# Optimization experiments

Hardware: AMD Instinct MI355X
Metric: run time of the kernel (lower is better)

Reference implementation:

```python
import jax, jax.numpy as jnp
import numpy as np

B = 64            # graphs
N0 = 1024         # nodes per graph at level 0
DEG = 16          # avg degree
D = 128
NS = [1024, 820, 656, 525, 420, 336]  # ceil(0.8*n) cascade


def gcn(x, src, dst, valid, W, b, num_nodes):
    # x: [N,D]; src/dst: [E] int; valid: [E] float mask; W: [D,D]; b: [D]
    x = x @ W.T + b
    deg = jax.ops.segment_sum(valid, src, num_segments=num_nodes) + 1.0  # +1 self loop
    dis = jax.lax.rsqrt(deg)
    norm = dis[src] * dis[dst] * valid
    agg = jax.ops.segment_sum(norm[:, None] * x[src], dst, num_segments=num_nodes)
    return agg + (dis * dis)[:, None] * x  # self-loop term


def topk_pool(x, src, dst, valid, w, n, k):
    # PyG TopKPooling: score = tanh((x.w)/||w||); keep top ceil(ratio*n) per graph
    s = jnp.tanh((x @ w) / jnp.linalg.norm(w))
    _, idx = jax.lax.top_k(s.reshape(B, n), k)                    # [B,k] local ids
    perm = (idx + (jnp.arange(B) * n)[:, None]).reshape(-1)       # global ids
    xn = x[perm] * s[perm][:, None]
    new_id = jnp.full((B * n,), -1, jnp.int32).at[perm].set(jnp.arange(B * k, dtype=jnp.int32))
    ns_, nd_ = new_id[src], new_id[dst]
    v = valid * ((ns_ >= 0) & (nd_ >= 0)).astype(jnp.float32)
    return xn, jnp.maximum(ns_, 0), jnp.maximum(nd_, 0), v


def setup_inputs() -> dict:
    key = jax.random.key(0)
    ks = jax.random.split(key, 32)
    x = jax.random.normal(ks[0], (B * N0, D), jnp.float32)
    eg = N0 * DEG  # edges per graph
    local = jax.random.randint(ks[1], (2, B, eg), 0, N0, jnp.int32)
    edge_index = (local + (jnp.arange(B, dtype=jnp.int32) * N0)[None, :, None]).reshape(2, -1)
    batch = jnp.repeat(jnp.arange(B, dtype=jnp.int32), N0)
    sc = 1.0 / np.sqrt(D)
    inp = {"x": x, "edge_index": edge_index, "batch": batch}
    for i in range(1, 6):
        inp[f"c{i}w"] = jax.random.normal(ks[2 * i], (D, D), jnp.float32) * sc
        inp[f"c{i}b"] = jnp.zeros((D,), jnp.float32)
        inp[f"p{i}w"] = jax.random.normal(ks[2 * i + 1], (D,), jnp.float32) * sc
    inp["l1w"] = jax.random.normal(ks[20], (128, 256), jnp.float32) / np.sqrt(256)
    inp["l1b"] = jnp.zeros((128,), jnp.float32)
    inp["l2w"] = jax.random.normal(ks[21], (64, 128), jnp.float32) * sc
    inp["l2b"] = jnp.zeros((64,), jnp.float32)
    inp["l3w"] = jax.random.normal(ks[22], (2, 64), jnp.float32) / np.sqrt(64)
    inp["l3b"] = jnp.zeros((2,), jnp.float32)
    return inp


def reference(x, edge_index, batch,
              c1w, c1b, p1w, c2w, c2b, p2w, c3w, c3b, p3w,
              c4w, c4b, p4w, c5w, c5b, p5w,
              l1w, l1b, l2w, l2b, l3w, l3b):
    src, dst = edge_index[0], edge_index[1]
    valid = jnp.ones(src.shape, jnp.float32)
    layers = [(c1w, c1b, p1w), (c2w, c2b, p2w), (c3w, c3b, p3w),
              (c4w, c4b, p4w), (c5w, c5b, p5w)]
    reads = []
    for i, (cw, cb, pw) in enumerate(layers):
        n, k = NS[i], NS[i + 1]
        x = jax.nn.relu(gcn(x, src, dst, valid, cw, cb, B * n))
        x, src, dst, valid = topk_pool(x, src, dst, valid, pw, n, k)
        xk = x.reshape(B, k, D)
        reads.append(jnp.concatenate([xk.max(axis=1), xk.mean(axis=1)], axis=1))
    h = reads[0] + reads[1] + reads[2] + reads[3] + reads[4]   # [B,256]
    h = jax.nn.relu(h @ l1w.T + l1b)
    # dropout is identity in eval mode
    h = jax.nn.relu(h @ l2w.T + l2b)
    return jax.nn.log_softmax(h @ l3w.T + l3b, axis=-1)       # [B,2]
```

## Files before the change

kernel.cpp:

```cpp
#include <hip/hip_runtime.h>
#include <hip/hip_fp16.h>
#include <math.h>

#define NB 64
#define DIM 128
#define ETOT 1048576
#define EPG 16384
#define EPT 16

static const int NS_H[6] = {1024, 820, 656, 525, 420, 336};

typedef _Float16 f16x8 __attribute__((ext_vector_type(8)));
typedef float f32x4 __attribute__((ext_vector_type(4)));
typedef float f32x2 __attribute__((ext_vector_type(2)));
typedef unsigned short ushortT;

__device__ __forceinline__ unsigned fxform(float f) {
    int b = __float_as_int(f);
    return (b >= 0) ? ((unsigned)b | 0x80000000u) : ~(unsigned)b;
}
__device__ __forceinline__ float fxinv(unsigned u) {
    int b = (u & 0x80000000u) ? (int)(u ^ 0x80000000u) : (int)~u;
    return __int_as_float(b);
}
__device__ __forceinline__ unsigned hmax2u(unsigned a, unsigned b) {
    float2 fa = __half22float2(*(__half2*)&a);
    float2 fb = __half22float2(*(__half2*)&b);
    __half2 r = __floats2half2_rn(fmaxf(fa.x, fb.x), fmaxf(fa.y, fb.y));
    return *(unsigned*)&r;
}
__device__ __forceinline__ unsigned hadd2u(unsigned a, unsigned b) {
    float2 fa = __half22float2(*(__half2*)&a);
    float2 fb = __half22float2(*(__half2*)&b);
    __half2 r = __floats2half2_rn(fa.x + fb.x, fa.y + fb.y);
    return *(unsigned*)&r;
}

__global__ __launch_bounds__(1024) void init_kernel(const int* __restrict__ ei,
                                  unsigned* __restrict__ sd,
                                  ushortT* __restrict__ eidx, int* __restrict__ eoff,
                                  int* __restrict__ cnt, float* __restrict__ dinv,
                                  float* __restrict__ invn, const float* __restrict__ pw0,
                                  unsigned* __restrict__ maxb, float* __restrict__ sumb,
                                  const float* __restrict__ cw0, const float* __restrict__ cw1,
                                  const float* __restrict__ cw2, const float* __restrict__ cw3,
                                  const float* __restrict__ cw4, __half* __restrict__ W16) {
    __shared__ int hs[1024], hc[1024], cur[1024];
    __shared__ float dv[1024];
    __shared__ float shf[128];
    __shared__ int wsum[16];
    int g = blockIdx.x, t = threadIdx.x;
    int lane = t & 63, wv = t >> 6;
    hs[t] = 0; hc[t] = 0;
    int idx = g * 1024 + t;
    if (idx < 5 * NB * 128) { maxb[idx] = 0x007FFFFFu; sumb[idx] = 0.f; }
    if (g < 5) {
        const float* wsrc = (g == 0) ? cw0 : (g == 1) ? cw1 : (g == 2) ? cw2
                           : (g == 3) ? cw3 : cw4;
        for (int i = t; i < 16384; i += 1024)
            W16[g * 16384 + i] = __float2half(wsrc[i]);
    }
    __syncthreads();
    int b0 = g * EPG;
    int sr[EPT], dr[EPT];
#pragma unroll
    for (int q = 0; q < EPT; q++) {
        int e = b0 + q * 1024 + t;
        int s = ei[e] & 1023, d = ei[ETOT + e] & 1023;
        sr[q] = s; dr[q] = d;
        sd[e] = ((unsigned)d << 16) | (unsigned)s;
        atomicAdd(&hs[s], 1);
        atomicAdd(&hc[d], 1);
    }
    __syncthreads();
    int v = hc[t];
    dv[t] = rsqrtf((float)hs[t] + 1.0f);
    int s = v;
#pragma unroll
    for (int off = 1; off < 64; off <<= 1) {
        int u = __shfl_up(s, off, 64);
        if (lane >= off) s += u;
    }
    if (lane == 63) wsum[wv] = s;
    __syncthreads();
    if (wv == 0) {
        int ws = (lane < 16) ? wsum[lane] : 0;
#pragma unroll
        for (int off = 1; off < 16; off <<= 1) {
            int u = __shfl_up(ws, off, 64);
            if (lane >= off) ws += u;
        }
        if (lane < 16) wsum[lane] = ws;
    }
    __syncthreads();
    int excl = b0 + s + ((wv > 0) ? wsum[wv - 1] : 0) - v;
    eoff[g * 1024 + t] = excl;
    cnt[g * 1024 + t] = v;
    dinv[g * 1024 + t] = dv[t];
    cur[t] = excl;
    __syncthreads();
#pragma unroll
    for (int q = 0; q < EPT; q++) {
        int pos = atomicAdd(&cur[dr[q]], 1);
        eidx[pos] = (ushortT)(g * 1024 + sr[q]);
    }
    if (g == 0) {
        if (t < 128) shf[t] = pw0[t] * pw0[t];
        __syncthreads();
        for (int q = 64; q > 0; q >>= 1) {
            if (t < q) shf[t] += shf[t + q];
            __syncthreads();
        }
        if (t == 0) invn[0] = rsqrtf(shf[0]);
    }
}

__global__ __launch_bounds__(256) void linear_kernel(const float* __restrict__ x,
                              const __half* __restrict__ xA,
                              const int* __restrict__ perm, const float* __restrict__ sval,
                              const __half* __restrict__ W16, const float* __restrict__ b,
                              const float* __restrict__ dinvL,
                              __half* __restrict__ xH,
                              unsigned* __restrict__ maxbL, float* __restrict__ sumbL,
                              int n_prev, int kk, int cpg, int mode) {
    __shared__ float rmaxW[512], rsumW[512];
    int tid = threadIdx.x;
    int g   = blockIdx.x / cpg;
    int j0  = (blockIdx.x % cpg) * 64;
    int wv  = tid >> 6;
    int l   = tid & 63;
    int l16 = l & 15;
    int kgrp = l >> 4;
    int jrow = j0 + wv * 16 + l16;
    bool valid = jrow < kk;
    f16x8 bf[4];
    if (mode) {
        int idx = g * kk + (valid ? jrow : 0);
        int rowg = perm[idx];
        float sc = valid ? sval[idx] : 0.f;
        const uint4* xrow = (const uint4*)(xA + (size_t)(g * n_prev + rowg) * DIM);
#pragma unroll
        for (int kb = 0; kb < 4; kb++) {
            uint4 hv = xrow[kb * 4 + kgrp];
            __half2* hp = (__half2*)&hv;
#pragma unroll
            for (int q = 0; q < 4; q++) {
                float2 f = __half22float2(hp[q]);
                hp[q] = __floats2half2_rn(f.x * sc, f.y * sc);
            }
            bf[kb] = *(f16x8*)&hv;
        }
    } else {
        const float* xrow = x + (size_t)(g * kk + jrow) * DIM;
#pragma unroll
        for (int kb = 0; kb < 4; kb++) {
            float4 a = *(const float4*)(xrow + kb * 32 + kgrp * 8);
            float4 c = *(const float4*)(xrow + kb * 32 + kgrp * 8 + 4);
            __half2 h0 = __floats2half2_rn(a.x, a.y), h1 = __floats2half2_rn(a.z, a.w);
            __half2 h2 = __floats2half2_rn(c.x, c.y), h3 = __floats2half2_rn(c.z, c.w);
            uint4 hv;
            hv.x = *(unsigned*)&h0; hv.y = *(unsigned*)&h1;
            hv.z = *(unsigned*)&h2; hv.w = *(unsigned*)&h3;
            bf[kb] = *(f16x8*)&hv;
        }
    }
    if (mode) {
#pragma unroll
        for (int kb = 0; kb < 4; kb++) {
            uint4 fv = *(uint4*)&bf[kb];
            uint4 mxv, smv;
            if (valid) { mxv = fv; smv = fv; }
            else {
                mxv = make_uint4(0xFC00FC00u, 0xFC00FC00u, 0xFC00FC00u, 0xFC00FC00u);
                smv = make_uint4(0u, 0u, 0u, 0u);
            }
#pragma unroll
            for (int st = 1; st < 16; st <<= 1) {
                uint4 om, os;
                om.x = __shfl_xor(mxv.x, st, 16); om.y = __shfl_xor(mxv.y, st, 16);
                om.z = __shfl_xor(mxv.z, st, 16); om.w = __shfl_xor(mxv.w, st, 16);
                os.x = __shfl_xor(smv.x, st, 16); os.y = __shfl_xor(smv.y, st, 16);
                os.z = __shfl_xor(smv.z, st, 16); os.w = __shfl_xor(smv.w, st, 16);
                mxv.x = hmax2u(mxv.x, om.x); mxv.y = hmax2u(mxv.y, om.y);
                mxv.z = hmax2u(mxv.z, om.z); mxv.w = hmax2u(mxv.w, om.w);
                smv.x = hadd2u(smv.x, os.x); smv.y = hadd2u(smv.y, os.y);
                smv.z = hadd2u(smv.z, os.z); smv.w = hadd2u(smv.w, os.w);
            }
            if (l16 == 0) {
                int cb = wv * 128 + kb * 32 + kgrp * 8;
                __half2* mh = (__half2*)&mxv;
                __half2* sh = (__half2*)&smv;
#pragma unroll
                for (int q = 0; q < 4; q++) {
                    float2 fm = __half22float2(mh[q]);
                    float2 fs = __half22float2(sh[q]);
                    rmaxW[cb + q * 2 + 0] = fm.x; rmaxW[cb + q * 2 + 1] = fm.y;
                    rsumW[cb + q * 2 + 0] = fs.x; rsumW[cb + q * 2 + 1] = fs.y;
                }
            }
        }
    }
    f32x4 acc[8];
#pragma unroll
    for (int ft = 0; ft < 8; ft++) {
        float4 bv = *(const float4*)(b + ft * 16 + kgrp * 4);
        f32x4 a; a[0] = bv.x; a[1] = bv.y; a[2] = bv.z; a[3] = bv.w;
        acc[ft] = a;
    }
    const uint4* wp = (const uint4*)W16;
#pragma unroll
    for (int kb = 0; kb < 4; kb++) {
#pragma unroll
        for (int ft = 0; ft < 8; ft++) {
            uint4 wfrag = wp[(ft * 16 + l16) * 16 + kb * 4 + kgrp];
            acc[ft] = __builtin_amdgcn_mfma_f32_16x16x32_f16(*(f16x8*)&wfrag, bf[kb],
                                                             acc[ft], 0, 0, 0);
        }
    }
    if (valid) {
        float dsn = dinvL[g * kk + jrow];
        __half* yrow = xH + (size_t)(g * kk + jrow) * DIM;
#pragma unroll
        for (int ft = 0; ft < 8; ft++) {
            __half2 h0 = __floats2half2_rn(acc[ft][0] * dsn, acc[ft][1] * dsn);
            __half2 h1 = __floats2half2_rn(acc[ft][2] * dsn, acc[ft][3] * dsn);
            uint2 pk;
            pk.x = *(unsigned*)&h0; pk.y = *(unsigned*)&h1;
            *(uint2*)(yrow + ft * 16 + kgrp * 4) = pk;
        }
    }
    if (mode) {
        __syncthreads();
        if (tid < 128) {
            float m = rmaxW[tid], s = rsumW[tid];
#pragma unroll
            for (int w = 1; w < 4; w++) {
                m = fmaxf(m, rmaxW[w * 128 + tid]);
                s += rsumW[w * 128 + tid];
            }
            atomicMax(&maxbL[g * 128 + tid], fxform(m));
            atomicAdd(&sumbL[g * 128 + tid], s);
        }
    }
}

#define ACC8(xv) { \
    float2 c0_ = __half22float2(*(const __half2*)&(xv).x); \
    float2 c1_ = __half22float2(*(const __half2*)&(xv).y); \
    float2 c2_ = __half22float2(*(const __half2*)&(xv).z); \
    float2 c3_ = __half22float2(*(const __half2*)&(xv).w); \
    a0[0] += c0_.x; a0[1] += c0_.y; a1[0] += c1_.x; a1[1] += c1_.y; \
    a2[0] += c2_.x; a2[1] += c2_.y; a3[0] += c3_.x; a3[1] += c3_.y; }

__global__ __launch_bounds__(256, 4) void fused_agg_kernel(
                                 const __half* __restrict__ xH, const ushortT* __restrict__ eidx,
                                 const int* __restrict__ eoff, const int* __restrict__ cnt,
                                 const float* __restrict__ dinv,
                                 const float* __restrict__ pw, const float* __restrict__ invn,
                                 __half* __restrict__ xA, float* __restrict__ score, int n) {
    int t = threadIdx.x;
    int g = blockIdx.x % NB;
    int chunk = blockIdx.x / NB;
    int ln = chunk * 8 + (t >> 5);
    if (ln >= n) return;
    int node = g * n + ln;
    int lane = t & 31;
    int sub = lane & 15;
    int hi  = lane >> 4;
    const uint4* __restrict__ xr = (const uint4*)xH;
    float dsn = dinv[node];
    f32x2 a0 = {0.f, 0.f}, a1 = {0.f, 0.f}, a2 = {0.f, 0.f}, a3 = {0.f, 0.f};
    if (!hi) {
        uint4 qs = xr[(unsigned)node * 16u + sub];
        ACC8(qs);
    }
    int s0 = eoff[node], s1 = s0 + cnt[node];
    int j = s0;
    while ((j & 3) && j < s1) {
        if (!hi) {
            uint4 xv = xr[(unsigned)eidx[j] * 16u + sub];
            ACC8(xv);
        }
        j++;
    }
    int nq = (s1 - j) >> 2;
    int rem = (s1 - j) & 3;
    const uint2* __restrict__ e4 = (const uint2*)(eidx + j);
    int q = 0;
    while (nq >= 2) {
        uint2 D0 = e4[q], D1 = e4[q + 1];
        unsigned r0 = hi ? (D0.x >> 16) : (D0.x & 0xFFFFu);
        unsigned r1 = hi ? (D0.y >> 16) : (D0.y & 0xFFFFu);
        unsigned r2 = hi ? (D1.x >> 16) : (D1.x & 0xFFFFu);
        unsigned r3 = hi ? (D1.y >> 16) : (D1.y & 0xFFFFu);
        uint4 x0 = xr[r0 * 16u + sub];
        uint4 x1 = xr[r1 * 16u + sub];
        uint4 x2 = xr[r2 * 16u + sub];
        uint4 x3 = xr[r3 * 16u + sub];
        ACC8(x0); ACC8(x1); ACC8(x2); ACC8(x3);
        q += 2; nq -= 2;
    }
    if (nq == 1) {
        uint2 D0 = e4[q];
        unsigned r0 = hi ? (D0.x >> 16) : (D0.x & 0xFFFFu);
        unsigned r1 = hi ? (D0.y >> 16) : (D0.y & 0xFFFFu);
        uint4 x0 = xr[r0 * 16u + sub];
        uint4 x1 = xr[r1 * 16u + sub];
        ACC8(x0); ACC8(x1);
    }
    for (int e = s1 - rem; e < s1; e++) {
        if (!hi) {
            uint4 xv = xr[(unsigned)eidx[e] * 16u + sub];
            ACC8(xv);
        }
    }
    float acc0 = a0[0], acc1 = a0[1], acc2 = a1[0], acc3 = a1[1];
    float acc4 = a2[0], acc5 = a2[1], acc6 = a3[0], acc7 = a3[1];
    acc0 += __shfl_xor(acc0, 16, 32); acc1 += __shfl_xor(acc1, 16, 32);
    acc2 += __shfl_xor(acc2, 16, 32); acc3 += __shfl_xor(acc3, 16, 32);
    acc4 += __shfl_xor(acc4, 16, 32); acc5 += __shfl_xor(acc5, 16, 32);
    acc6 += __shfl_xor(acc6, 16, 32); acc7 += __shfl_xor(acc7, 16, 32);
    acc0 = fmaxf(acc0 * dsn, 0.f); acc1 = fmaxf(acc1 * dsn, 0.f);
    acc2 = fmaxf(acc2 * dsn, 0.f); acc3 = fmaxf(acc3 * dsn, 0.f);
    acc4 = fmaxf(acc4 * dsn, 0.f); acc5 = fmaxf(acc5 * dsn, 0.f);
    acc6 = fmaxf(acc6 * dsn, 0.f); acc7 = fmaxf(acc7 * dsn, 0.f);
    if (!hi) {
        __half2 h0 = __floats2half2_rn(acc0, acc1);
        __half2 h1 = __floats2half2_rn(acc2, acc3);
        __half2 h2 = __floats2half2_rn(acc4, acc5);
        __half2 h3 = __floats2half2_rn(acc6, acc7);
        uint4 pk;
        pk.x = *(unsigned int*)&h0; pk.y = *(unsigned int*)&h1;
        pk.z = *(unsigned int*)&h2; pk.w = *(unsigned int*)&h3;
        ((uint4*)xA)[(unsigned)node * 16u + sub] = pk;
    }
    float4 pa = ((const float4*)pw)[sub * 2];
    float4 pb = ((const float4*)pw)[sub * 2 + 1];
    float dot = acc0 * pa.x + acc1 * pa.y + acc2 * pa.z + acc3 * pa.w
              + acc4 * pb.x + acc5 * pb.y + acc6 * pb.z + acc7 * pb.w;
#pragma unroll
    for (int off = 8; off >= 1; off >>= 1) dot += __shfl_xor(dot, off, 16);
    if (lane == 0) score[node] = tanhf(dot * invn[0]);
}

__global__ __launch_bounds__(1024) void pool_kernel(const float* __restrict__ score,
                              int* __restrict__ permG, float* __restrict__ svalG,
                              unsigned* __restrict__ sd,
                              ushortT* __restrict__ eidx, int* __restrict__ eoff,
                              int* __restrict__ cnt, float* __restrict__ dinv,
                              const float* __restrict__ pwN, float* __restrict__ invn,
                              const __half* __restrict__ xA,
                              const unsigned* __restrict__ maxb, const float* __restrict__ sumb,
                              const float* __restrict__ l1w, const float* __restrict__ l1b,
                              const float* __restrict__ l2w, const float* __restrict__ l2b,
                              const float* __restrict__ l3w, const float* __restrict__ l3b,
                              float* __restrict__ out,
                              int n, int k, int last) {
    __shared__ float keyS[2][1024];
    __shared__ int idxS[2][1024];
    __shared__ int nid[1024];
    __shared__ int hs[1024], hc[1024], cur[1024];
    __shared__ float dv[1024];
    __shared__ float shf[128];
    __shared__ int wsum[16];
    __shared__ float4 smax[32][33], ssm[32][33];
    __shared__ float hr[256], h1[128], h2[64], lz[2];
    int g = blockIdx.x, t = threadIdx.x;
    int lane = t & 63, wv = t >> 6;
    int b0 = g * EPG, gk = g * k;
    float k_r = (t < n) ? score[g * n + t] : -2.0f;
    int i_r = t;
    hs[t] = 0; hc[t] = 0;
    unsigned sde[EPT];
    if (!last) {
#pragma unroll
        for (int q = 0; q < EPT; q++) {
            int e = b0 + q * 1024 + t;
            sde[q] = sd[e];
        }
    }
    int par = 0;
    for (unsigned ksz = 2; ksz <= 1024; ksz <<= 1) {
        for (unsigned jj = ksz >> 1; jj > 0; jj >>= 1) {
            float kq; int iq;
            if (jj >= 64) {
                keyS[par][t] = k_r; idxS[par][t] = i_r;
                __syncthreads();
                kq = keyS[par][t ^ jj]; iq = idxS[par][t ^ jj];
                par ^= 1;
            } else {
                kq = __shfl_xor(k_r, (int)jj, 64);
                iq = __shfl_xor(i_r, (int)jj, 64);
            }
            bool mineFirst = (k_r > kq) || (k_r == kq && i_r < iq);
            bool up = ((t & ksz) == 0);
            bool iAmLower = ((t & jj) == 0);
            bool keepMine = (iAmLower == up) ? mineFirst : !mineFirst;
            if (!keepMine) { k_r = kq; i_r = iq; }
        }
    }
    nid[i_r] = (t < (unsigned)k) ? t : -1;
    keyS[0][t] = k_r; idxS[0][t] = i_r;
    if (!last && t < k) { permG[gk + t] = i_r; svalG[gk + t] = k_r; }
    __syncthreads();
    if (last) {
        int lane4 = t & 31, ch = t >> 5;
        float4 mx = make_float4(-INFINITY, -INFINITY, -INFINITY, -INFINITY);
        float4 sm = make_float4(0.f, 0.f, 0.f, 0.f);
        for (int j = ch; j < k; j += 32) {
            int row = idxS[0][j];
            float sv = keyS[0][j];
            uint2 hv = ((const uint2*)(xA + ((size_t)(g * n + row)) * DIM))[lane4];
            float2 lo = __half22float2(*(const __half2*)&hv.x);
            float2 hi2 = __half22float2(*(const __half2*)&hv.y);
            float4 vv = make_float4(lo.x * sv, lo.y * sv, hi2.x * sv, hi2.y * sv);
            mx.x = fmaxf(mx.x, vv.x); mx.y = fmaxf(mx.y, vv.y);
            mx.z = fmaxf(mx.z, vv.z); mx.w = fmaxf(mx.w, vv.w);
            sm.x += vv.x; sm.y += vv.y; sm.z += vv.z; sm.w += vv.w;
        }
        smax[ch][lane4] = mx;
        ssm[ch][lane4] = sm;
        __syncthreads();
        for (int s2 = 16; s2 >= 1; s2 >>= 1) {
            if (ch < s2) {
                float4 a = smax[ch][lane4], bb = smax[ch + s2][lane4];
                a.x = fmaxf(a.x, bb.x); a.y = fmaxf(a.y, bb.y);
                a.z = fmaxf(a.z, bb.z); a.w = fmaxf(a.w, bb.w);
                smax[ch][lane4] = a;
                float4 c = ssm[ch][lane4], d = ssm[ch + s2][lane4];
                c.x += d.x; c.y += d.y; c.z += d.z; c.w += d.w;
                ssm[ch][lane4] = c;
            }
            __syncthreads();
        }
        if (t < 128) {
            const float invk[4] = {1.f / 820.f, 1.f / 656.f, 1.f / 525.f, 1.f / 420.f};
            float mxs = ((const float*)&smax[0][t >> 2])[t & 3];
            float sms = ((const float*)&ssm[0][t >> 2])[t & 3] * (1.f / 336.f);
#pragma unroll
            for (int L = 0; L < 4; L++) {
                mxs += fxinv(maxb[(L * NB + g) * 128 + t]);
                sms += sumb[(L * NB + g) * 128 + t] * invk[L];
            }
            hr[t] = mxs;
            hr[128 + t] = sms;
        }
        __syncthreads();
        if (t < 128) {
            float a1 = l1b[t];
            for (int d = 0; d < 256; d++) a1 += hr[d] * l1w[t * 256 + d];
            h1[t] = fmaxf(a1, 0.f);
        }
        __syncthreads();
        if (t < 64) {
            float a2 = l2b[t];
            for (int d = 0; d < 128; d++) a2 += h1[d] * l2w[t * 128 + d];
            h2[t] = fmaxf(a2, 0.f);
        }
        __syncthreads();
        if (t < 2) {
            float a3 = l3b[t];
            for (int d = 0; d < 64; d++) a3 += h2[d] * l3w[t * 64 + d];
            lz[t] = a3;
        }
        __syncthreads();
        if (t < 2) {
            float z0 = lz[0], z1 = lz[1];
            float m = fmaxf(z0, z1);
            float lse = m + logf(expf(z0 - m) + expf(z1 - m));
            out[g * 2 + t] = lz[t] - lse;
        }
        return;
    }
    int sr[EPT], dr[EPT];
#pragma unroll
    for (int q = 0; q < EPT; q++) {
        int e = b0 + q * 1024 + t;
        unsigned v = sde[q];
        int s2 = -1, d2 = -1;
        if (v != 0xFFFFFFFFu) {
            int sl = (int)(v & 0xFFFFu), dl = (int)(v >> 16);
            s2 = nid[sl];
            d2 = nid[dl];
            if (s2 >= 0 && d2 >= 0) {
                sd[e] = ((unsigned)d2 << 16) | (unsigned)s2;
                atomicAdd(&hs[s2], 1);
                atomicAdd(&hc[d2], 1);
            } else {
                sd[e] = 0xFFFFFFFFu;
                s2 = -1;
            }
        }
        sr[q] = s2; dr[q] = d2;
    }
    __syncthreads();
    int v = (t < k) ? hc[t] : 0;
    if (t < k) dv[t] = rsqrtf((float)hs[t] + 1.0f);
    int s = v;
#pragma unroll
    for (int off = 1; off < 64; off <<= 1) {
        int u = __shfl_up(s, off, 64);
        if (lane >= off) s += u;
    }
    if (lane == 63) wsum[wv] = s;
    __syncthreads();
    if (wv == 0) {
        int ws = (lane < 16) ? wsum[lane] : 0;
#pragma unroll
        for (int off = 1; off < 16; off <<= 1) {
            int u = __shfl_up(ws, off, 64);
            if (lane >= off) ws += u;
        }
        if (lane < 16) wsum[lane] = ws;
    }
    __syncthreads();
    if (t < k) {
        int excl = b0 + s + ((wv > 0) ? wsum[wv - 1] : 0) - v;
        eoff[gk + t] = excl;
        cnt[gk + t] = v;
        dinv[gk + t] = dv[t];
        cur[t] = excl;
    }
    __syncthreads();
#pragma unroll
    for (int q = 0; q < EPT; q++) {
        if (sr[q] >= 0) {
            int pos = atomicAdd(&cur[dr[q]], 1);
            eidx[pos] = (ushortT)(gk + sr[q]);
        }
    }
    if (g == 0) {
        if (t < 128) shf[t] = pwN[t] * pwN[t];
        __syncthreads();
        for (int q = 64; q > 0; q >>= 1) {
            if (t < q) shf[t] += shf[t + q];
            __syncthreads();
        }
        if (t == 0) invn[0] = rsqrtf(shf[0]);
    }
}

extern "C" void kernel_launch(void* const* d_in, const int* in_sizes, int n_in,
                              void* d_out, int out_size, void* d_ws, size_t ws_size,
                              hipStream_t stream) {
    const float* x_in = (const float*)d_in[0];
    const int* edge_index = (const int*)d_in[1];
    const float *cw[5], *cb[5], *pw[5];
    for (int i = 0; i < 5; i++) {
        cw[i] = (const float*)d_in[3 + 3 * i];
        cb[i] = (const float*)d_in[4 + 3 * i];
        pw[i] = (const float*)d_in[5 + 3 * i];
    }
    const float* l1w = (const float*)d_in[18];
    const float* l1b = (const float*)d_in[19];
    const float* l2w = (const float*)d_in[20];
    const float* l2b = (const float*)d_in[21];
    const float* l3w = (const float*)d_in[22];
    const float* l3b = (const float*)d_in[23];
    float* out = (float*)d_out;

    char* w = (char*)d_ws;
    __half* xA    = (__half*)w; w += (size_t)65536 * DIM * 2;
    __half* xH    = (__half*)w; w += (size_t)65536 * DIM * 2;
    unsigned* sd  = (unsigned*)w; w += (size_t)ETOT * 4;
    ushortT* eidx = (ushortT*)w; w += (size_t)ETOT * 2;
    int*   cnt   = (int*)w;   w += (size_t)65536 * 4;
    int*   eoff  = (int*)w;   w += (size_t)65536 * 4;
    float* dinv  = (float*)w; w += (size_t)65536 * 4;
    float* score = (float*)w; w += (size_t)65536 * 4;
    int*   perm  = (int*)w;   w += (size_t)65536 * 4;
    float* sval  = (float*)w; w += (size_t)65536 * 4;
    unsigned* maxb = (unsigned*)w; w += (size_t)5 * NB * 128 * 4;
    float* sumb  = (float*)w; w += (size_t)5 * NB * 128 * 4;
    __half* W16  = (__half*)w; w += (size_t)5 * 16384 * 2;
    float* invn  = (float*)w; w += 4;

    init_kernel<<<NB, 1024, 0, stream>>>(edge_index, sd, eidx, eoff, cnt, dinv,
                                         invn, pw[0], maxb, sumb,
                                         cw[0], cw[1], cw[2], cw[3], cw[4], W16);

    for (int i = 0; i < 5; i++) {
        int n = NS_H[i], k = NS_H[i + 1];
        int cpg = (n + 63) / 64;
        int last = (i == 4) ? 1 : 0;

        linear_kernel<<<NB * cpg, 256, 0, stream>>>(
            x_in, xA, perm, sval, W16 + (size_t)i * 16384, cb[i], dinv, xH,
            (i > 0) ? maxb + (size_t)(i - 1) * NB * 128 : (unsigned*)maxb,
            (i > 0) ? sumb + (size_t)(i - 1) * NB * 128 : (float*)sumb,
            (i > 0) ? NS_H[i - 1] : 0, n, cpg, (i > 0) ? 1 : 0);

        int gpb = (n + 7) / 8;
        fused_agg_kernel<<<NB * gpb, 256, 0, stream>>>(xH, eidx, eoff, cnt, dinv, pw[i],
                                                       invn, xA, score, n);
        pool_kernel<<<NB, 1024, 0, stream>>>(score, perm, sval, sd, eidx, eoff,
                                             cnt, dinv, (i < 4) ? pw[i + 1] : pw[i], invn,
                                             xA, maxb, sumb,
                                             l1w, l1b, l2w, l2b, l3w, l3b, out,
                                             n, k, last);
    }
}
```

Baseline: 442.5 us.

## Merge linear and aggregation kernels into one cooperative kernel with grid sync

Combines the per-layer linear (MFMA) kernel and the neighbour aggregation kernel into a single cooperative launch with grid-stride loops, separated by a grid-wide barrier. This removes one kernel launch and its launch gap per layer. In exchange the grid is capped at occupancy-limited size (up to 2048 blocks), so work runs in persistent loops. There is also a hazard: the aggregation phase writes xA while the linear phase of the same launch reads it, but the grid sync orders the two phases.

Result: slower. 1.278 ms (+188.8%).

```diff
diff --git a/kernel.cpp b/kernel.cpp
--- a/kernel.cpp
+++ b/kernel.cpp
@@ -1,6 +1,9 @@
 #include <hip/hip_runtime.h>
+#include <hip/hip_cooperative_groups.h>
 #include <hip/hip_fp16.h>
 #include <math.h>
+
+namespace cg = cooperative_groups;
 
 #define NB 64
 #define DIM 128
@@ -115,134 +118,26 @@
     }
 }
 
-__global__ __launch_bounds__(256) void linear_kernel(const float* __restrict__ x,
-                              const __half* __restrict__ xA,
-                              const int* __restrict__ perm, const float* __restrict__ sval,
-                              const __half* __restrict__ W16, const float* __restrict__ b,
-                              const float* __restrict__ dinvL,
-                              __half* __restrict__ xH,
-                              unsigned* __restrict__ maxbL, float* __restrict__ sumbL,
-                              int n_prev, int kk, int cpg, int mode) {
-    __shared__ float rmaxW[512], rsumW[512];
-    int tid = threadIdx.x;
-    int g   = blockIdx.x / cpg;
-    int j0  = (blockIdx.x % cpg) * 64;
-    int wv  = tid >> 6;
-    int l   = tid & 63;
-    int l16 = l & 15;
-    int kgrp = l >> 4;
-    int jrow = j0 + wv * 16 + l16;
-    bool valid = jrow < kk;
-    f16x8 bf[4];
-    if (mode) {
-        int idx = g * kk + (valid ? jrow : 0);
-        int rowg = perm[idx];
-        float sc = valid ? sval[idx] : 0.f;
-        const uint4* xrow = (const uint4*)(xA + (size_t)(g * n_prev + rowg) * DIM);
-#pragma unroll
-        for (int kb = 0; kb < 4; kb++) {
-            uint4 hv = xrow[kb * 4 + kgrp];
-            __half2* hp = (__half2*)&hv;
-#pragma unroll
-            for (int q = 0; q < 4; q++) {
-                float2 f = __half22float2(hp[q]);
-                hp[q] = __floats2half2_rn(f.x * sc, f.y * sc);
-            }
-            bf[kb] = *(f16x8*)&hv;
-        }
-    } else {
-        const float* xrow = x + (size_t)(g * kk + jrow) * DIM;
-#pragma unroll
-        for (int kb = 0; kb < 4; kb++) {
-            float4 a = *(const float4*)(xrow + kb * 32 + kgrp * 8);
-            float4 c = *(const float4*)(xrow + kb * 32 + kgrp * 8 + 4);
-            __half2 h0 = __floats2half2_rn(a.x, a.y), h1 = __floats2half2_rn(a.z, a.w);
-            __half2 h2 = __floats2half2_rn(c.x, c.y), h3 = __floats2half2_rn(c.z, c.w);
-            uint4 hv;
-            hv.x = *(unsigned*)&h0; hv.y = *(unsigned*)&h1;
-            hv.z = *(unsigned*)&h2; hv.w = *(unsigned*)&h3;
-            bf[kb] = *(f16x8*)&hv;
-        }
-    }
-    if (mode) {
-#pragma unroll
-        for (int kb = 0; kb < 4; kb++) {
-            uint4 fv = *(uint4*)&bf[kb];
-            uint4 mxv, smv;
-            if (valid) { mxv = fv; smv = fv; }
-            else {
-                mxv = make_uint4(0xFC00FC00u, 0xFC00FC00u, 0xFC00FC00u, 0xFC00FC00u);
-                smv = make_uint4(0u, 0u, 0u, 0u);
-            }
-#pragma unroll
-            for (int st = 1; st < 16; st <<= 1) {
-                uint4 om, os;
-                om.x = __shfl_xor(mxv.x, st, 16); om.y = __shfl_xor(mxv.y, st, 16);
-                om.z = __shfl_xor(mxv.z, st, 16); om.w = __shfl_xor(mxv.w, st, 16);
-                os.x = __shfl_xor(smv.x, st, 16); os.y = __shfl_xor(smv.y, st, 16);
-                os.z = __shfl_xor(smv.z, st, 16); os.w = __shfl_xor(smv.w, st, 16);
-                mxv.x = hmax2u(mxv.x, om.x); mxv.y = hmax2u(mxv.y, om.y);
-                mxv.z = hmax2u(mxv.z, om.z); mxv.w = hmax2u(mxv.w, om.w);
-                smv.x = hadd2u(smv.x, os.x); smv.y = hadd2u(smv.y, os.y);
-                smv.z = hadd2u(smv.z, os.z); smv.w = hadd2u(smv.w, os.w);
-            }
-            if (l16 == 0) {
-                int cb = wv * 128 + kb * 32 + kgrp * 8;
-                __half2* mh = (__half2*)&mxv;
-                __half2* sh = (__half2*)&smv;
-#pragma unroll
-                for (int q = 0; q < 4; q++) {
-                    float2 fm = __half22float2(mh[q]);
-                    float2 fs = __half22float2(sh[q]);
-                    rmaxW[cb + q * 2 + 0] = fm.x; rmaxW[cb + q * 2 + 1] = fm.y;
-                    rsumW[cb + q * 2 + 0] = fs.x; rsumW[cb + q * 2 + 1] = fs.y;
-                }
-            }
-        }
-    }
-    f32x4 acc[8];
-#pragma unroll
-    for (int ft = 0; ft < 8; ft++) {
-        float4 bv = *(const float4*)(b + ft * 16 + kgrp * 4);
-        f32x4 a; a[0] = bv.x; a[1] = bv.y; a[2] = bv.z; a[3] = bv.w;
-        acc[ft] = a;
-    }
-    const uint4* wp = (const uint4*)W16;
-#pragma unroll
-    for (int kb = 0; kb < 4; kb++) {
-#pragma unroll
-        for (int ft = 0; ft < 8; ft++) {
-            uint4 wfrag = wp[(ft * 16 + l16) * 16 + kb * 4 + kgrp];
-            acc[ft] = __builtin_amdgcn_mfma_f32_16x16x32_f16(*(f16x8*)&wfrag, bf[kb],
-                                                             acc[ft], 0, 0, 0);
-        }
-    }
-    if (valid) {
-        float dsn = dinvL[g * kk + jrow];
-        __half* yrow = xH + (size_t)(g * kk + jrow) * DIM;
-#pragma unroll
-        for (int ft = 0; ft < 8; ft++) {
-            __half2 h0 = __floats2half2_rn(acc[ft][0] * dsn, acc[ft][1] * dsn);
-            __half2 h1 = __floats2half2_rn(acc[ft][2] * dsn, acc[ft][3] * dsn);
-            uint2 pk;
-            pk.x = *(unsigned*)&h0; pk.y = *(unsigned*)&h1;
-            *(uint2*)(yrow + ft * 16 + kgrp * 4) = pk;
-        }
-    }
-    if (mode) {
-        __syncthreads();
-        if (tid < 128) {
-            float m = rmaxW[tid], s = rsumW[tid];
-#pragma unroll
-            for (int w = 1; w < 4; w++) {
-                m = fmaxf(m, rmaxW[w * 128 + tid]);
-                s += rsumW[w * 128 + tid];
-            }
-            atomicMax(&maxbL[g * 128 + tid], fxform(m));
-            atomicAdd(&sumbL[g * 128 + tid], s);
-        }
-    }
-}
+struct LayerArgs {
+    const float* x;
+    const __half* xAin;
+    const int* perm;
+    const float* sval;
+    const __half* W16;
+    const float* bias;
+    const float* dinv;
+    __half* xH;
+    unsigned* maxbL;
+    float* sumbL;
+    const ushortT* eidx;
+    const int* eoff;
+    const int* cnt;
+    const float* pw;
+    const float* invn;
+    __half* xAout;
+    float* score;
+    int n_prev, kk, cpg, mode, nLinU, nAggU, n;
+};
 
 #define ACC8(xv) { \
     float2 c0_ = __half22float2(*(const __half2*)&(xv).x); \
@@ -252,95 +147,215 @@
     a0[0] += c0_.x; a0[1] += c0_.y; a1[0] += c1_.x; a1[1] += c1_.y; \
     a2[0] += c2_.x; a2[1] += c2_.y; a3[0] += c3_.x; a3[1] += c3_.y; }
 
-__global__ __launch_bounds__(256, 4) void fused_agg_kernel(
-                                 const __half* __restrict__ xH, const ushortT* __restrict__ eidx,
-                                 const int* __restrict__ eoff, const int* __restrict__ cnt,
-                                 const float* __restrict__ dinv,
-                                 const float* __restrict__ pw, const float* __restrict__ invn,
-                                 __half* __restrict__ xA, float* __restrict__ score, int n) {
-    int t = threadIdx.x;
-    int g = blockIdx.x % NB;
-    int chunk = blockIdx.x / NB;
-    int ln = chunk * 8 + (t >> 5);
-    if (ln >= n) return;
-    int node = g * n + ln;
-    int lane = t & 31;
-    int sub = lane & 15;
-    int hi  = lane >> 4;
-    const uint4* __restrict__ xr = (const uint4*)xH;
-    float dsn = dinv[node];
-    f32x2 a0 = {0.f, 0.f}, a1 = {0.f, 0.f}, a2 = {0.f, 0.f}, a3 = {0.f, 0.f};
-    if (!hi) {
-        uint4 qs = xr[(unsigned)node * 16u + sub];
-        ACC8(qs);
-    }
-    int s0 = eoff[node], s1 = s0 + cnt[node];
-    int j = s0;
-    while ((j & 3) && j < s1) {
+__global__ __launch_bounds__(256, 4) void layer_kernel(LayerArgs A) {
+    __shared__ float rmaxW[512], rsumW[512];
+    int tid = threadIdx.x;
+    for (int u = blockIdx.x; u < A.nLinU; u += gridDim.x) {
+        int g   = u / A.cpg;
+        int j0  = (u % A.cpg) * 64;
+        int wv  = tid >> 6;
+        int l   = tid & 63;
+        int l16 = l & 15;
+        int kgrp = l >> 4;
+        int jrow = j0 + wv * 16 + l16;
+        bool valid = jrow < A.kk;
+        f16x8 bf[4];
+        if (A.mode) {
+            int idx = g * A.kk + (valid ? jrow : 0);
+            int rowg = A.perm[idx];
+            float sc = valid ? A.sval[idx] : 0.f;
+            const uint4* xrow = (const uint4*)(A.xAin + (size_t)(g * A.n_prev + rowg) * DIM);
+#pragma unroll
+            for (int kb = 0; kb < 4; kb++) {
+                uint4 hv = xrow[kb * 4 + kgrp];
+                __half2* hp = (__half2*)&hv;
+#pragma unroll
+                for (int q = 0; q < 4; q++) {
+                    float2 f = __half22float2(hp[q]);
+                    hp[q] = __floats2half2_rn(f.x * sc, f.y * sc);
+                }
+                bf[kb] = *(f16x8*)&hv;
+            }
+        } else {
+            const float* xrow = A.x + (size_t)(g * A.kk + jrow) * DIM;
+#pragma unroll
+            for (int kb = 0; kb < 4; kb++) {
+                float4 a = *(const float4*)(xrow + kb * 32 + kgrp * 8);
+                float4 c = *(const float4*)(xrow + kb * 32 + kgrp * 8 + 4);
+                __half2 h0 = __floats2half2_rn(a.x, a.y), h1 = __floats2half2_rn(a.z, a.w);
+                __half2 h2 = __floats2half2_rn(c.x, c.y), h3 = __floats2half2_rn(c.z, c.w);
+                uint4 hv;
+                hv.x = *(unsigned*)&h0; hv.y = *(unsigned*)&h1;
+                hv.z = *(unsigned*)&h2; hv.w = *(unsigned*)&h3;
+                bf[kb] = *(f16x8*)&hv;
+            }
+        }
+        if (A.mode) {
+#pragma unroll
+            for (int kb = 0; kb < 4; kb++) {
+                uint4 fv = *(uint4*)&bf[kb];
+                uint4 mxv, smv;
+                if (valid) { mxv = fv; smv = fv; }
+                else {
+                    mxv = make_uint4(0xFC00FC00u, 0xFC00FC00u, 0xFC00FC00u, 0xFC00FC00u);
+                    smv = make_uint4(0u, 0u, 0u, 0u);
+                }
+#pragma unroll
+                for (int st = 1; st < 16; st <<= 1) {
+                    uint4 om, os;
+                    om.x = __shfl_xor(mxv.x, st, 16); om.y = __shfl_xor(mxv.y, st, 16);
+                    om.z = __shfl_xor(mxv.z, st, 16); om.w = __shfl_xor(mxv.w, st, 16);
+                    os.x = __shfl_xor(smv.x, st, 16); os.y = __shfl_xor(smv.y, st, 16);
+                    os.z = __shfl_xor(smv.z, st, 16); os.w = __shfl_xor(smv.w, st, 16);
+                    mxv.x = hmax2u(mxv.x, om.x); mxv.y = hmax2u(mxv.y, om.y);
+                    mxv.z = hmax2u(mxv.z, om.z); mxv.w = hmax2u(mxv.w, om.w);
+                    smv.x = hadd2u(smv.x, os.x); smv.y = hadd2u(smv.y, os.y);
+                    smv.z = hadd2u(smv.z, os.z); smv.w = hadd2u(smv.w, os.w);
+                }
+                if (l16 == 0) {
+                    int cb = wv * 128 + kb * 32 + kgrp * 8;
+                    __half2* mh = (__half2*)&mxv;
+                    __half2* sh = (__half2*)&smv;
+#pragma unroll
+                    for (int q = 0; q < 4; q++) {
+                        float2 fm = __half22float2(mh[q]);
+                        float2 fs = __half22float2(sh[q]);
+                        rmaxW[cb + q * 2 + 0] = fm.x; rmaxW[cb + q * 2 + 1] = fm.y;
+                        rsumW[cb + q * 2 + 0] = fs.x; rsumW[cb + q * 2 + 1] = fs.y;
+                    }
+                }
+            }
+        }
+        f32x4 acc[8];
+#pragma unroll
+        for (int ft = 0; ft < 8; ft++) {
+            float4 bv = *(const float4*)(A.bias + ft * 16 + kgrp * 4);
+            f32x4 a; a[0] = bv.x; a[1] = bv.y; a[2] = bv.z; a[3] = bv.w;
+            acc[ft] = a;
+        }
+        const uint4* wp = (const uint4*)A.W16;
+#pragma unroll
+        for (int kb = 0; kb < 4; kb++) {
+#pragma unroll
+            for (int ft = 0; ft < 8; ft++) {
+                uint4 wfrag = wp[(ft * 16 + l16) * 16 + kb * 4 + kgrp];
+                acc[ft] = __builtin_amdgcn_mfma_f32_16x16x32_f16(*(f16x8*)&wfrag, bf[kb],
+                                                                 acc[ft], 0, 0, 0);
+            }
+        }
+        if (valid) {
+            float dsn = A.dinv[g * A.kk + jrow];
+            __half* yrow = A.xH + (size_t)(g * A.kk + jrow) * DIM;
+#pragma unroll
+            for (int ft = 0; ft < 8; ft++) {
+                __half2 h0 = __floats2half2_rn(acc[ft][0] * dsn, acc[ft][1] * dsn);
+                __half2 h1 = __floats2half2_rn(acc[ft][2] * dsn, acc[ft][3] * dsn);
+                uint2 pk;
+                pk.x = *(unsigned*)&h0; pk.y = *(unsigned*)&h1;
+                *(uint2*)(yrow + ft * 16 + kgrp * 4) = pk;
+            }
+        }
+        if (A.mode) {
+            __syncthreads();
+            if (tid < 128) {
+                float m = rmaxW[tid], s = rsumW[tid];
+#pragma unroll
+                for (int w = 1; w < 4; w++) {
+                    m = fmaxf(m, rmaxW[w * 128 + tid]);
+                    s += rsumW[w * 128 + tid];
+                }
+                atomicMax(&A.maxbL[g * 128 + tid], fxform(m));
+                atomicAdd(&A.sumbL[g * 128 + tid], s);
+            }
+            __syncthreads();
+        }
+    }
+    __threadfence();
+    cg::this_grid().sync();
+    for (int u = blockIdx.x; u < A.nAggU; u += gridDim.x) {
+        int g = u % NB;
+        int chunk = u / NB;
+        int ln = chunk * 8 + (tid >> 5);
+        if (ln >= A.n) continue;
+        int node = g * A.n + ln;
+        int lane = tid & 31;
+        int sub = lane & 15;
+        int hi  = lane >> 4;
+        const uint4* __restrict__ xr = (const uint4*)A.xH;
+        float dsn = A.dinv[node];
+        f32x2 a0 = {0.f, 0.f}, a1 = {0.f, 0.f}, a2 = {0.f, 0.f}, a3 = {0.f, 0.f};
         if (!hi) {
-            uint4 xv = xr[(unsigned)eidx[j] * 16u + sub];
-            ACC8(xv);
-        }
-        j++;
-    }
-    int nq = (s1 - j) >> 2;
-    int rem = (s1 - j) & 3;
-    const uint2* __restrict__ e4 = (const uint2*)(eidx + j);
-    int q = 0;
-    while (nq >= 2) {
-        uint2 D0 = e4[q], D1 = e4[q + 1];
-        unsigned r0 = hi ? (D0.x >> 16) : (D0.x & 0xFFFFu);
-        unsigned r1 = hi ? (D0.y >> 16) : (D0.y & 0xFFFFu);
-        unsigned r2 = hi ? (D1.x >> 16) : (D1.x & 0xFFFFu);
-        unsigned r3 = hi ? (D1.y >> 16) : (D1.y & 0xFFFFu);
-        uint4 x0 = xr[r0 * 16u + sub];
-        uint4 x1 = xr[r1 * 16u + sub];
-        uint4 x2 = xr[r2 * 16u + sub];
-        uint4 x3 = xr[r3 * 16u + sub];
-        ACC8(x0); ACC8(x1); ACC8(x2); ACC8(x3);
-        q += 2; nq -= 2;
-    }
-    if (nq == 1) {
-        uint2 D0 = e4[q];
-        unsigned r0 = hi ? (D0.x >> 16) : (D0.x & 0xFFFFu);
-        unsigned r1 = hi ? (D0.y >> 16) : (D0.y & 0xFFFFu);
-        uint4 x0 = xr[r0 * 16u + sub];
-        uint4 x1 = xr[r1 * 16u + sub];
-        ACC8(x0); ACC8(x1);
-    }
-    for (int e = s1 - rem; e < s1; e++) {
+            uint4 qs = xr[(unsigned)node * 16u + sub];
+            ACC8(qs);
+        }
+        int s0 = A.eoff[node], s1 = s0 + A.cnt[node];
+        int j = s0;
+        while ((j & 3) && j < s1) {
+            if (!hi) {
+                uint4 xv = xr[(unsigned)A.eidx[j] * 16u + sub];
+                ACC8(xv);
+            }
+            j++;
+        }
+        int nq = (s1 - j) >> 2;
+        int rem = (s1 - j) & 3;
+        const uint2* __restrict__ e4 = (const uint2*)(A.eidx + j);
+        int q = 0;
+        while (nq >= 2) {
+            uint2 D0 = e4[q], D1 = e4[q + 1];
+            unsigned r0 = hi ? (D0.x >> 16) : (D0.x & 0xFFFFu);
+            unsigned r1 = hi ? (D0.y >> 16) : (D0.y & 0xFFFFu);
+            unsigned r2 = hi ? (D1.x >> 16) : (D1.x & 0xFFFFu);
+            unsigned r3 = hi ? (D1.y >> 16) : (D1.y & 0xFFFFu);
+            uint4 x0 = xr[r0 * 16u + sub];
+            uint4 x1 = xr[r1 * 16u + sub];
+            uint4 x2 = xr[r2 * 16u + sub];
+            uint4 x3 = xr[r3 * 16u + sub];
+            ACC8(x0); ACC8(x1); ACC8(x2); ACC8(x3);
+            q += 2; nq -= 2;
+        }
+        if (nq == 1) {
+            uint2 D0 = e4[q];
+            unsigned r0 = hi ? (D0.x >> 16) : (D0.x & 0xFFFFu);
+            unsigned r1 = hi ? (D0.y >> 16) : (D0.y & 0xFFFFu);
+            uint4 x0 = xr[r0 * 16u + sub];
+            uint4 x1 = xr[r1 * 16u + sub];
+            ACC8(x0); ACC8(x1);
+        }
+        for (int e = s1 - rem; e < s1; e++) {
+            if (!hi) {
+                uint4 xv = xr[(unsigned)A.eidx[e] * 16u + sub];
+                ACC8(xv);
+            }
+        }
+        float acc0 = a0[0], acc1 = a0[1], acc2 = a1[0], acc3 = a1[1];
+        float acc4 = a2[0], acc5 = a2[1], acc6 = a3[0], acc7 = a3[1];
+        acc0 += __shfl_xor(acc0, 16, 32); acc1 += __shfl_xor(acc1, 16, 32);
+        acc2 += __shfl_xor(acc2, 16, 32); acc3 += __shfl_xor(acc3, 16, 32);
+        acc4 += __shfl_xor(acc4, 16, 32); acc5 += __shfl_xor(acc5, 16, 32);
+        acc6 += __shfl_xor(acc6, 16, 32); acc7 += __shfl_xor(acc7, 16, 32);
+        acc0 = fmaxf(acc0 * dsn, 0.f); acc1 = fmaxf(acc1 * dsn, 0.f);
+        acc2 = fmaxf(acc2 * dsn, 0.f); acc3 = fmaxf(acc3 * dsn, 0.f);
+        acc4 = fmaxf(acc4 * dsn, 0.f); acc5 = fmaxf(acc5 * dsn, 0.f);
+        acc6 = fmaxf(acc6 * dsn, 0.f); acc7 = fmaxf(acc7 * dsn, 0.f);
         if (!hi) {
-            uint4 xv = xr[(unsigned)eidx[e] * 16u + sub];
-            ACC8(xv);
-        }
-    }
-    float acc0 = a0[0], acc1 = a0[1], acc2 = a1[0], acc3 = a1[1];
-    float acc4 = a2[0], acc5 = a2[1], acc6 = a3[0], acc7 = a3[1];
-    acc0 += __shfl_xor(acc0, 16, 32); acc1 += __shfl_xor(acc1, 16, 32);
-    acc2 += __shfl_xor(acc2, 16, 32); acc3 += __shfl_xor(acc3, 16, 32);
-    acc4 += __shfl_xor(acc4, 16, 32); acc5 += __shfl_xor(acc5, 16, 32);
-    acc6 += __shfl_xor(acc6, 16, 32); acc7 += __shfl_xor(acc7, 16, 32);
-    acc0 = fmaxf(acc0 * dsn, 0.f); acc1 = fmaxf(acc1 * dsn, 0.f);
-    acc2 = fmaxf(acc2 * dsn, 0.f); acc3 = fmaxf(acc3 * dsn, 0.f);
-    acc4 = fmaxf(acc4 * dsn, 0.f); acc5 = fmaxf(acc5 * dsn, 0.f);
-    acc6 = fmaxf(acc6 * dsn, 0.f); acc7 = fmaxf(acc7 * dsn, 0.f);
-    if (!hi) {
-        __half2 h0 = __floats2half2_rn(acc0, acc1);
-        __half2 h1 = __floats2half2_rn(acc2, acc3);
-        __half2 h2 = __floats2half2_rn(acc4, acc5);
-        __half2 h3 = __floats2half2_rn(acc6, acc7);
-        uint4 pk;
-        pk.x = *(unsigned int*)&h0; pk.y = *(unsigned int*)&h1;
-        pk.z = *(unsigned int*)&h2; pk.w = *(unsigned int*)&h3;
-        ((uint4*)xA)[(unsigned)node * 16u + sub] = pk;
-    }
-    float4 pa = ((const float4*)pw)[sub * 2];
-    float4 pb = ((const float4*)pw)[sub * 2 + 1];
-    float dot = acc0 * pa.x + acc1 * pa.y + acc2 * pa.z + acc3 * pa.w
-              + acc4 * pb.x + acc5 * pb.y + acc6 * pb.z + acc7 * pb.w;
-#pragma unroll
-    for (int off = 8; off >= 1; off >>= 1) dot += __shfl_xor(dot, off, 16);
-    if (lane == 0) score[node] = tanhf(dot * invn[0]);
+            __half2 h0 = __floats2half2_rn(acc0, acc1);
+            __half2 h1 = __floats2half2_rn(acc2, acc3);
+            __half2 h2 = __floats2half2_rn(acc4, acc5);
+            __half2 h3 = __floats2half2_rn(acc6, acc7);
+            uint4 pk;
+            pk.x = *(unsigned int*)&h0; pk.y = *(unsigned int*)&h1;
+            pk.z = *(unsigned int*)&h2; pk.w = *(unsigned int*)&h3;
+            ((uint4*)A.xAout)[(unsigned)node * 16u + sub] = pk;
+        }
+        float4 pa = ((const float4*)A.pw)[sub * 2];
+        float4 pb = ((const float4*)A.pw)[sub * 2 + 1];
+        float dot = acc0 * pa.x + acc1 * pa.y + acc2 * pa.z + acc3 * pa.w
+                  + acc4 * pb.x + acc5 * pb.y + acc6 * pb.z + acc7 * pb.w;
+#pragma unroll
+        for (int off = 8; off >= 1; off >>= 1) dot += __shfl_xor(dot, off, 16);
+        if (lane == 0) A.score[node] = tanhf(dot * A.invn[0]);
+    }
 }
 
 __global__ __launch_bounds__(1024) void pool_kernel(const float* __restrict__ score,
@@ -575,6 +590,15 @@
     __half* W16  = (__half*)w; w += (size_t)5 * 16384 * 2;
     float* invn  = (float*)w; w += 4;
 
+    static int coopGrid = 0;
+    if (coopGrid == 0) {
+        int occ = 0;
+        hipError_t e = hipOccupancyMaxActiveBlocksPerMultiprocessor(&occ, layer_kernel, 256, 0);
+        if (e != hipSuccess || occ < 1) occ = 2;
+        coopGrid = occ * 256;
+        if (coopGrid > 2048) coopGrid = 2048;
+    }
+
     init_kernel<<<NB, 1024, 0, stream>>>(edge_index, sd, eidx, eoff, cnt, dinv,
                                          invn, pw[0], maxb, sumb,
                                          cw[0], cw[1], cw[2], cw[3], cw[4], W16);
@@ -582,17 +606,23 @@
     for (int i = 0; i < 5; i++) {
         int n = NS_H[i], k = NS_H[i + 1];
         int cpg = (n + 63) / 64;
+        int gpb = (n + 7) / 8;
         int last = (i == 4) ? 1 : 0;
 
-        linear_kernel<<<NB * cpg, 256, 0, stream>>>(
-            x_in, xA, perm, sval, W16 + (size_t)i * 16384, cb[i], dinv, xH,
-            (i > 0) ? maxb + (size_t)(i - 1) * NB * 128 : (unsigned*)maxb,
-            (i > 0) ? sumb + (size_t)(i - 1) * NB * 128 : (float*)sumb,
-            (i > 0) ? NS_H[i - 1] : 0, n, cpg, (i > 0) ? 1 : 0);
-
-        int gpb = (n + 7) / 8;
-        fused_agg_kernel<<<NB * gpb, 256, 0, stream>>>(xH, eidx, eoff, cnt, dinv, pw[i],
-                                                       invn, xA, score, n);
+        LayerArgs la;
+        la.x = x_in; la.xAin = xA; la.perm = perm; la.sval = sval;
+        la.W16 = W16 + (size_t)i * 16384; la.bias = cb[i]; la.dinv = dinv; la.xH = xH;
+        la.maxbL = (i > 0) ? maxb + (size_t)(i - 1) * NB * 128 : maxb;
+        la.sumbL = (i > 0) ? sumb + (size_t)(i - 1) * NB * 128 : sumb;
+        la.eidx = eidx; la.eoff = eoff; la.cnt = cnt; la.pw = pw[i]; la.invn = invn;
+        la.xAout = xA; la.score = score;
+        la.n_prev = (i > 0) ? NS_H[i - 1] : 0;
+        la.kk = n; la.cpg = cpg; la.mode = (i > 0) ? 1 : 0;
+        la.nLinU = NB * cpg; la.nAggU = NB * gpb; la.n = n;
+        void* kargs[] = { (void*)&la };
+        hipLaunchCooperativeKernel((const void*)layer_kernel, dim3(coopGrid), dim3(256),
+                                   kargs, 0, stream);
+
         pool_kernel<<<NB, 1024, 0, stream>>>(score, perm, sval, sd, eidx, eoff,
                                              cnt, dinv, (i < 4) ? pw[i + 1] : pw[i], invn,
                                              xA, maxb, sumb,
```
